# Optimization experiments

Hardware: AMD Instinct MI355X
Metric: run time of the kernel (lower is better)

Reference implementation:

```python
import jax, jax.numpy as jnp
import numpy as np

H = 64  # hidden size
IN = 4  # input size


def _lstm_cell(h, c, xt, w_ih, w_hh, b):
    # PyTorch gate order: i, f, g, o
    gates = xt @ w_ih.T + h @ w_hh.T + b  # [B, 4H]
    i, f, g, o = jnp.split(gates, 4, axis=-1)
    i = jax.nn.sigmoid(i)
    f = jax.nn.sigmoid(f)
    g = jnp.tanh(g)
    o = jax.nn.sigmoid(o)
    c = f * c + i * g
    h = o * jnp.tanh(c)
    return h, c


def setup_inputs() -> dict:
    key = jax.random.key(0)
    ks = jax.random.split(key, 12)
    B, T = 512, 1000
    s = 1.0 / np.sqrt(H)  # PyTorch LSTM/Linear init scale
    u = lambda k, shape: jax.random.uniform(k, shape, jnp.float32, -s, s)
    return {
        "x": jax.random.normal(ks[0], (B, T, IN), jnp.float32),
        "w_ih_f": u(ks[1], (4 * H, IN)),
        "w_hh_f": u(ks[2], (4 * H, H)),
        "b_ih_f": u(ks[3], (4 * H,)),
        "b_hh_f": u(ks[4], (4 * H,)),
        "w_ih_b": u(ks[5], (4 * H, IN)),
        "w_hh_b": u(ks[6], (4 * H, H)),
        "b_ih_b": u(ks[7], (4 * H,)),
        "b_hh_b": u(ks[8], (4 * H,)),
        "w_fc": u(ks[9], (1, 2 * H)),
        "b_fc": u(ks[10], (1,)),
    }


def reference(x, w_ih_f, w_hh_f, b_ih_f, b_hh_f,
              w_ih_b, w_hh_b, b_ih_b, b_hh_b, w_fc, b_fc):
    B = x.shape[0]
    # Forward-direction LSTM: only the final hidden state is consumed
    # (out[:, -1, :64] == h_fwd after the last step).
    b_f = b_ih_f + b_hh_f

    def step(carry, xt):
        h, c = carry
        h, c = _lstm_cell(h, c, xt, w_ih_f, w_hh_f, b_f)
        return (h, c), None

    init = (jnp.zeros((B, H), x.dtype), jnp.zeros((B, H), x.dtype))
    xs = jnp.swapaxes(x, 0, 1)  # [T, B, IN]
    (h_fwd, _), _ = jax.lax.scan(step, init, xs)

    # Backward-direction output at the LAST timestep is the backward LSTM's
    # FIRST step (it processes the sequence reversed from zero state):
    # out[:, -1, 64:] == cell(0, 0, x[:, -1]).
    b_b = b_ih_b + b_hh_b
    h0 = jnp.zeros((B, H), x.dtype)
    h_bwd, _ = _lstm_cell(h0, h0, x[:, -1, :], w_ih_b, w_hh_b, b_b)

    last = jnp.concatenate([h_fwd, h_bwd], axis=-1)  # [B, 128]
    # Dropout is identity in eval mode.
    logits = last @ w_fc.T + b_fc  # [B, 1]
    return jax.nn.sigmoid(logits)[:, 0]
```

## Files before the change

### kernel.cpp

```cpp
#include <hip/hip_runtime.h>

#define HDIM 64

typedef _Float16 h2  __attribute__((ext_vector_type(2)));
typedef __fp16   fp2 __attribute__((ext_vector_type(2)));

#if defined(__has_builtin)
# if __has_builtin(__builtin_amdgcn_fdot2)
#  define FDOT2(a, b, c) __builtin_amdgcn_fdot2((a), (b), (c), false)
# endif
#endif
#ifndef FDOT2
__device__ __forceinline__ float fdot2_asm(h2 a, h2 b, float c) {
    float d;
    asm("v_dot2_f32_f16 %0, %1, %2, %3" : "=v"(d) : "v"(a), "v"(b), "v"(c));
    return d;
}
# define FDOT2(a, b, c) fdot2_asm((a), (b), (c))
#endif

__device__ __forceinline__ float fast_sigmoid(float v) {
    return __builtin_amdgcn_rcpf(1.0f + __builtin_amdgcn_exp2f(-1.442695041f * v));
}

__device__ __forceinline__ float fast_tanh(float v) {
    return 1.0f - 2.0f * __builtin_amdgcn_rcpf(1.0f + __builtin_amdgcn_exp2f(2.885390082f * v));
}

__global__ __launch_bounds__(64)
__attribute__((amdgpu_waves_per_eu(1, 1)))
void bilstm_kernel(const float* __restrict__ x,
                   const float* __restrict__ w_ih_f,
                   const float* __restrict__ w_hh_f,
                   const float* __restrict__ b_ih_f,
                   const float* __restrict__ b_hh_f,
                   const float* __restrict__ w_ih_b,
                   const float* __restrict__ b_ih_b,
                   const float* __restrict__ b_hh_b,
                   const float* __restrict__ w_fc,
                   const float* __restrict__ b_fc,
                   float* __restrict__ out,
                   int T)
{
    const int b = blockIdx.x;
    const int l = threadIdx.x;

    __shared__ __align__(16) _Float16 hlds[HDIM];

    unsigned wu[128];
    #pragma unroll
    for (int g = 0; g < 4; ++g) {
        const float* row = w_hh_f + (size_t)((g << 6) | l) * HDIM;
        #pragma unroll
        for (int q = 0; q < 16; ++q) {
            float4 v = *(const float4*)(row + 4 * q);
            fp2 p0 = __builtin_amdgcn_cvt_pkrtz(v.x, v.y);
            fp2 p1 = __builtin_amdgcn_cvt_pkrtz(v.z, v.w);
            wu[(g << 5) + 2 * q + 0] = __builtin_bit_cast(unsigned, p0);
            wu[(g << 5) + 2 * q + 1] = __builtin_bit_cast(unsigned, p1);
        }
    }
    #pragma unroll
    for (int q = 0; q < 16; ++q) {
        asm volatile("" : "+v"(wu[8*q+0]), "+v"(wu[8*q+1]),
                          "+v"(wu[8*q+2]), "+v"(wu[8*q+3]),
                          "+v"(wu[8*q+4]), "+v"(wu[8*q+5]),
                          "+v"(wu[8*q+6]), "+v"(wu[8*q+7]));
    }

    float4 wx[4];
    float  bz[4];
    #pragma unroll
    for (int g = 0; g < 4; ++g) {
        const int r = (g << 6) | l;
        wx[g] = *(const float4*)(w_ih_f + (size_t)r * 4);
        bz[g] = b_ih_f[r] + b_hh_f[r];
        asm volatile("" : "+v"(wx[g].x), "+v"(wx[g].y), "+v"(wx[g].z),
                          "+v"(wx[g].w), "+v"(bz[g]));
    }

    hlds[l] = (_Float16)0.0f;

    const float* xb = x + (size_t)b * T * 4;
    float4 xcur = *(const float4*)(xb);
    float c = 0.0f, h = 0.0f;

    #define W2(g, qq) __builtin_bit_cast(h2, wu[((g) << 5) + (qq)])
    #define H2(u)     __builtin_bit_cast(h2, (u))

    for (int t = 0; t < T; ++t) {
        const int tn = (t + 1 < T) ? t + 1 : T - 1;
        float4 xnext = *(const float4*)(xb + 4 * tn);

        float aA0 = bz[0], aB0 = 0.0f;
        float aA1 = bz[1], aB1 = 0.0f;
        float aA2 = bz[2], aB2 = 0.0f;
        float aA3 = bz[3], aB3 = 0.0f;

        const uint4* hp = (const uint4*)hlds;
        #pragma unroll
        for (int q = 0; q < 8; ++q) {
            const uint4 hv = hp[q];
            aA0 = FDOT2(W2(0, 4*q+0), H2(hv.x), aA0);
            aB0 = FDOT2(W2(0, 4*q+1), H2(hv.y), aB0);
            aA0 = FDOT2(W2(0, 4*q+2), H2(hv.z), aA0);
            aB0 = FDOT2(W2(0, 4*q+3), H2(hv.w), aB0);
            aA1 = FDOT2(W2(1, 4*q+0), H2(hv.x), aA1);
            aB1 = FDOT2(W2(1, 4*q+1), H2(hv.y), aB1);
            aA1 = FDOT2(W2(1, 4*q+2), H2(hv.z), aA1);
            aB1 = FDOT2(W2(1, 4*q+3), H2(hv.w), aB1);
            aA2 = FDOT2(W2(2, 4*q+0), H2(hv.x), aA2);
            aB2 = FDOT2(W2(2, 4*q+1), H2(hv.y), aB2);
            aA2 = FDOT2(W2(2, 4*q+2), H2(hv.z), aA2);
            aB2 = FDOT2(W2(2, 4*q+3), H2(hv.w), aB2);
            aA3 = FDOT2(W2(3, 4*q+0), H2(hv.x), aA3);
            aB3 = FDOT2(W2(3, 4*q+1), H2(hv.y), aB3);
            aA3 = FDOT2(W2(3, 4*q+2), H2(hv.z), aA3);
            aB3 = FDOT2(W2(3, 4*q+3), H2(hv.w), aB3);
        }

        float A0 = aA0 + aB0 + (wx[0].x * xcur.x + wx[0].y * xcur.y
                              + wx[0].z * xcur.z + wx[0].w * xcur.w);
        float A1 = aA1 + aB1 + (wx[1].x * xcur.x + wx[1].y * xcur.y
                              + wx[1].z * xcur.z + wx[1].w * xcur.w);
        float A2 = aA2 + aB2 + (wx[2].x * xcur.x + wx[2].y * xcur.y
                              + wx[2].z * xcur.z + wx[2].w * xcur.w);
        float A3 = aA3 + aB3 + (wx[3].x * xcur.x + wx[3].y * xcur.y
                              + wx[3].z * xcur.z + wx[3].w * xcur.w);

        const float gi = fast_sigmoid(A0);
        const float gf = fast_sigmoid(A1);
        const float gg = fast_tanh(A2);
        const float go = fast_sigmoid(A3);
        c = gf * c + gi * gg;
        h = go * fast_tanh(c);

        hlds[l] = (_Float16)h;
        asm volatile("" ::: "memory");
        xcur = xnext;
    }

    #undef W2
    #undef H2

    float gb[4];
    #pragma unroll
    for (int g = 0; g < 4; ++g) {
        const int r = (g << 6) | l;
        float4 wb = *(const float4*)(w_ih_b + (size_t)r * 4);
        gb[g] = b_ih_b[r] + b_hh_b[r]
              + wb.x * xcur.x + wb.y * xcur.y + wb.z * xcur.z + wb.w * xcur.w;
    }
    const float ib  = fast_sigmoid(gb[0]);
    const float ggb = fast_tanh(gb[2]);
    const float ob  = fast_sigmoid(gb[3]);
    const float cb  = ib * ggb;
    const float hb  = ob * fast_tanh(cb);

    float p = w_fc[l] * h + w_fc[HDIM + l] * hb;
    #pragma unroll
    for (int off = 32; off; off >>= 1) p += __shfl_xor(p, off);

    if (l == 0) out[b] = fast_sigmoid(p + b_fc[0]);
}

extern "C" void kernel_launch(void* const* d_in, const int* in_sizes, int n_in,
                              void* d_out, int out_size, void* d_ws, size_t ws_size,
                              hipStream_t stream) {
    const float* x      = (const float*)d_in[0];
    const float* w_ih_f = (const float*)d_in[1];
    const float* w_hh_f = (const float*)d_in[2];
    const float* b_ih_f = (const float*)d_in[3];
    const float* b_hh_f = (const float*)d_in[4];
    const float* w_ih_b = (const float*)d_in[5];
    const float* b_ih_b = (const float*)d_in[7];
    const float* b_hh_b = (const float*)d_in[8];
    const float* w_fc   = (const float*)d_in[9];
    const float* b_fc   = (const float*)d_in[10];
    float* out = (float*)d_out;

    const int B = out_size;
    const int T = in_sizes[0] / (B * 4);

    bilstm_kernel<<<dim3(B), dim3(64), 0, stream>>>(
        x, w_ih_f, w_hh_f, b_ih_f, b_hh_f,
        w_ih_b, b_ih_b, b_hh_b, w_fc, b_fc, out, T);
}
```

Baseline: 446.7 us.

## Process two batch sequences per wavefront to reuse register-resident weights

Each 64-thread block now runs two independent batch rows through the recurrence at once, sharing the fp16 recurrent weights held in registers, and the grid is halved. The two chains interleave, so one row's dependency latency (LDS read, dot products, transcendentals) can hide behind the other's work. The input projection also moves to packed fp16 dot products to save registers and instructions. The cost is fewer blocks (256 on a many-CU GPU, which leaves CUs idle), more per-thread instructions per step, higher register pressure, and lower input-projection precision.

Result: slower. 747.5 us (+67.4%).

```diff
diff --git a/kernel.cpp b/kernel.cpp
--- a/kernel.cpp
+++ b/kernel.cpp
@@ -42,10 +42,12 @@
                    float* __restrict__ out,
                    int T)
 {
-    const int b = blockIdx.x;
-    const int l = threadIdx.x;
-
-    __shared__ __align__(16) _Float16 hlds[HDIM];
+    const int b0 = 2 * blockIdx.x;
+    const int b1 = b0 + 1;
+    const int l  = threadIdx.x;
+
+    __shared__ __align__(16) _Float16 hlds0[HDIM];
+    __shared__ __align__(16) _Float16 hlds1[HDIM];
 
     unsigned wu[128];
     #pragma unroll
@@ -68,100 +70,136 @@
                           "+v"(wu[8*q+6]), "+v"(wu[8*q+7]));
     }
 
-    float4 wx[4];
-    float  bz[4];
+    unsigned wxu[8];
+    float    bz[4];
     #pragma unroll
     for (int g = 0; g < 4; ++g) {
         const int r = (g << 6) | l;
-        wx[g] = *(const float4*)(w_ih_f + (size_t)r * 4);
+        float4 v = *(const float4*)(w_ih_f + (size_t)r * 4);
+        fp2 p0 = __builtin_amdgcn_cvt_pkrtz(v.x, v.y);
+        fp2 p1 = __builtin_amdgcn_cvt_pkrtz(v.z, v.w);
+        wxu[2*g + 0] = __builtin_bit_cast(unsigned, p0);
+        wxu[2*g + 1] = __builtin_bit_cast(unsigned, p1);
         bz[g] = b_ih_f[r] + b_hh_f[r];
-        asm volatile("" : "+v"(wx[g].x), "+v"(wx[g].y), "+v"(wx[g].z),
-                          "+v"(wx[g].w), "+v"(bz[g]));
-    }
-
-    hlds[l] = (_Float16)0.0f;
-
-    const float* xb = x + (size_t)b * T * 4;
-    float4 xcur = *(const float4*)(xb);
-    float c = 0.0f, h = 0.0f;
+    }
+    asm volatile("" : "+v"(wxu[0]), "+v"(wxu[1]), "+v"(wxu[2]), "+v"(wxu[3]),
+                      "+v"(wxu[4]), "+v"(wxu[5]), "+v"(wxu[6]), "+v"(wxu[7]));
+    asm volatile("" : "+v"(bz[0]), "+v"(bz[1]), "+v"(bz[2]), "+v"(bz[3]));
+
+    hlds0[l] = (_Float16)0.0f;
+    hlds1[l] = (_Float16)0.0f;
+
+    const float* xb0 = x + (size_t)b0 * T * 4;
+    const float* xb1 = x + (size_t)b1 * T * 4;
+    float4 xc0 = *(const float4*)xb0;
+    float4 xc1 = *(const float4*)xb1;
+    float c0 = 0.0f, h0 = 0.0f, c1 = 0.0f, h1 = 0.0f;
 
     #define W2(g, qq) __builtin_bit_cast(h2, wu[((g) << 5) + (qq)])
+    #define WX2(k)    __builtin_bit_cast(h2, wxu[k])
     #define H2(u)     __builtin_bit_cast(h2, (u))
 
     for (int t = 0; t < T; ++t) {
         const int tn = (t + 1 < T) ? t + 1 : T - 1;
-        float4 xnext = *(const float4*)(xb + 4 * tn);
-
-        float aA0 = bz[0], aB0 = 0.0f;
-        float aA1 = bz[1], aB1 = 0.0f;
-        float aA2 = bz[2], aB2 = 0.0f;
-        float aA3 = bz[3], aB3 = 0.0f;
-
-        const uint4* hp = (const uint4*)hlds;
+        float4 xn0 = *(const float4*)(xb0 + 4 * tn);
+        float4 xn1 = *(const float4*)(xb1 + 4 * tn);
+
+        float accA[2][4], accB[2][4];
+        #pragma unroll
+        for (int g = 0; g < 4; ++g) {
+            accA[0][g] = bz[g]; accB[0][g] = 0.0f;
+            accA[1][g] = bz[g]; accB[1][g] = 0.0f;
+        }
+
+        const uint4* hp0 = (const uint4*)hlds0;
+        const uint4* hp1 = (const uint4*)hlds1;
         #pragma unroll
         for (int q = 0; q < 8; ++q) {
-            const uint4 hv = hp[q];
-            aA0 = FDOT2(W2(0, 4*q+0), H2(hv.x), aA0);
-            aB0 = FDOT2(W2(0, 4*q+1), H2(hv.y), aB0);
-            aA0 = FDOT2(W2(0, 4*q+2), H2(hv.z), aA0);
-            aB0 = FDOT2(W2(0, 4*q+3), H2(hv.w), aB0);
-            aA1 = FDOT2(W2(1, 4*q+0), H2(hv.x), aA1);
-            aB1 = FDOT2(W2(1, 4*q+1), H2(hv.y), aB1);
-            aA1 = FDOT2(W2(1, 4*q+2), H2(hv.z), aA1);
-            aB1 = FDOT2(W2(1, 4*q+3), H2(hv.w), aB1);
-            aA2 = FDOT2(W2(2, 4*q+0), H2(hv.x), aA2);
-            aB2 = FDOT2(W2(2, 4*q+1), H2(hv.y), aB2);
-            aA2 = FDOT2(W2(2, 4*q+2), H2(hv.z), aA2);
-            aB2 = FDOT2(W2(2, 4*q+3), H2(hv.w), aB2);
-            aA3 = FDOT2(W2(3, 4*q+0), H2(hv.x), aA3);
-            aB3 = FDOT2(W2(3, 4*q+1), H2(hv.y), aB3);
-            aA3 = FDOT2(W2(3, 4*q+2), H2(hv.z), aA3);
-            aB3 = FDOT2(W2(3, 4*q+3), H2(hv.w), aB3);
-        }
-
-        float A0 = aA0 + aB0 + (wx[0].x * xcur.x + wx[0].y * xcur.y
-                              + wx[0].z * xcur.z + wx[0].w * xcur.w);
-        float A1 = aA1 + aB1 + (wx[1].x * xcur.x + wx[1].y * xcur.y
-                              + wx[1].z * xcur.z + wx[1].w * xcur.w);
-        float A2 = aA2 + aB2 + (wx[2].x * xcur.x + wx[2].y * xcur.y
-                              + wx[2].z * xcur.z + wx[2].w * xcur.w);
-        float A3 = aA3 + aB3 + (wx[3].x * xcur.x + wx[3].y * xcur.y
-                              + wx[3].z * xcur.z + wx[3].w * xcur.w);
-
-        const float gi = fast_sigmoid(A0);
-        const float gf = fast_sigmoid(A1);
-        const float gg = fast_tanh(A2);
-        const float go = fast_sigmoid(A3);
-        c = gf * c + gi * gg;
-        h = go * fast_tanh(c);
-
-        hlds[l] = (_Float16)h;
+            const uint4 v0 = hp0[q];
+            const uint4 v1 = hp1[q];
+            #pragma unroll
+            for (int g = 0; g < 4; ++g) {
+                accA[0][g] = FDOT2(W2(g, 4*q+0), H2(v0.x), accA[0][g]);
+                accB[0][g] = FDOT2(W2(g, 4*q+1), H2(v0.y), accB[0][g]);
+                accA[0][g] = FDOT2(W2(g, 4*q+2), H2(v0.z), accA[0][g]);
+                accB[0][g] = FDOT2(W2(g, 4*q+3), H2(v0.w), accB[0][g]);
+                accA[1][g] = FDOT2(W2(g, 4*q+0), H2(v1.x), accA[1][g]);
+                accB[1][g] = FDOT2(W2(g, 4*q+1), H2(v1.y), accB[1][g]);
+                accA[1][g] = FDOT2(W2(g, 4*q+2), H2(v1.z), accA[1][g]);
+                accB[1][g] = FDOT2(W2(g, 4*q+3), H2(v1.w), accB[1][g]);
+            }
+        }
+
+        const unsigned x01_0 = __builtin_bit_cast(unsigned, __builtin_amdgcn_cvt_pkrtz(xc0.x, xc0.y));
+        const unsigned x23_0 = __builtin_bit_cast(unsigned, __builtin_amdgcn_cvt_pkrtz(xc0.z, xc0.w));
+        const unsigned x01_1 = __builtin_bit_cast(unsigned, __builtin_amdgcn_cvt_pkrtz(xc1.x, xc1.y));
+        const unsigned x23_1 = __builtin_bit_cast(unsigned, __builtin_amdgcn_cvt_pkrtz(xc1.z, xc1.w));
+
+        float pre[2][4];
+        #pragma unroll
+        for (int g = 0; g < 4; ++g) {
+            float t0 = accA[0][g] + accB[0][g];
+            t0 = FDOT2(WX2(2*g + 0), H2(x01_0), t0);
+            t0 = FDOT2(WX2(2*g + 1), H2(x23_0), t0);
+            pre[0][g] = t0;
+            float t1 = accA[1][g] + accB[1][g];
+            t1 = FDOT2(WX2(2*g + 0), H2(x01_1), t1);
+            t1 = FDOT2(WX2(2*g + 1), H2(x23_1), t1);
+            pre[1][g] = t1;
+        }
+
+        {
+            const float gi = fast_sigmoid(pre[0][0]);
+            const float gf = fast_sigmoid(pre[0][1]);
+            const float gg = fast_tanh(pre[0][2]);
+            const float go = fast_sigmoid(pre[0][3]);
+            c0 = gf * c0 + gi * gg;
+            h0 = go * fast_tanh(c0);
+        }
+        {
+            const float gi = fast_sigmoid(pre[1][0]);
+            const float gf = fast_sigmoid(pre[1][1]);
+            const float gg = fast_tanh(pre[1][2]);
+            const float go = fast_sigmoid(pre[1][3]);
+            c1 = gf * c1 + gi * gg;
+            h1 = go * fast_tanh(c1);
+        }
+
+        hlds0[l] = (_Float16)h0;
+        hlds1[l] = (_Float16)h1;
         asm volatile("" ::: "memory");
-        xcur = xnext;
+        xc0 = xn0;
+        xc1 = xn1;
     }
 
     #undef W2
+    #undef WX2
     #undef H2
 
-    float gb[4];
-    #pragma unroll
-    for (int g = 0; g < 4; ++g) {
-        const int r = (g << 6) | l;
-        float4 wb = *(const float4*)(w_ih_b + (size_t)r * 4);
-        gb[g] = b_ih_b[r] + b_hh_b[r]
-              + wb.x * xcur.x + wb.y * xcur.y + wb.z * xcur.z + wb.w * xcur.w;
-    }
-    const float ib  = fast_sigmoid(gb[0]);
-    const float ggb = fast_tanh(gb[2]);
-    const float ob  = fast_sigmoid(gb[3]);
-    const float cb  = ib * ggb;
-    const float hb  = ob * fast_tanh(cb);
-
-    float p = w_fc[l] * h + w_fc[HDIM + l] * hb;
-    #pragma unroll
-    for (int off = 32; off; off >>= 1) p += __shfl_xor(p, off);
-
-    if (l == 0) out[b] = fast_sigmoid(p + b_fc[0]);
+    #pragma unroll
+    for (int e = 0; e < 2; ++e) {
+        const float4 xl = e ? xc1 : xc0;
+        const float  hf = e ? h1 : h0;
+        float gb[4];
+        #pragma unroll
+        for (int g = 0; g < 4; ++g) {
+            const int r = (g << 6) | l;
+            float4 wb = *(const float4*)(w_ih_b + (size_t)r * 4);
+            gb[g] = b_ih_b[r] + b_hh_b[r]
+                  + wb.x * xl.x + wb.y * xl.y + wb.z * xl.z + wb.w * xl.w;
+        }
+        const float ib  = fast_sigmoid(gb[0]);
+        const float ggb = fast_tanh(gb[2]);
+        const float ob  = fast_sigmoid(gb[3]);
+        const float cb  = ib * ggb;
+        const float hbk = ob * fast_tanh(cb);
+
+        float p = w_fc[l] * hf + w_fc[HDIM + l] * hbk;
+        #pragma unroll
+        for (int off = 32; off; off >>= 1) p += __shfl_xor(p, off);
+
+        if (l == 0) out[e ? b1 : b0] = fast_sigmoid(p + b_fc[0]);
+    }
 }
 
 extern "C" void kernel_launch(void* const* d_in, const int* in_sizes, int n_in,
@@ -182,7 +220,7 @@
     const int B = out_size;
     const int T = in_sizes[0] / (B * 4);
 
-    bilstm_kernel<<<dim3(B), dim3(64), 0, stream>>>(
+    bilstm_kernel<<<dim3(B / 2), dim3(64), 0, stream>>>(
         x, w_ih_f, w_hh_f, b_ih_f, b_hh_f,
         w_ih_b, b_ih_b, b_hh_b, w_fc, b_fc, out, T);
 }
```
